# Kernel tuning notes

Measured on AMD Instinct MI355X. Metric: run time of the kernel, lower is better.

Reference implementation:

```python
import jax, jax.numpy as jnp
import numpy as np

L, CIN, CKV, E, H, D, NQ, NK = 3, 128, 256, 128, 8, 16, 4096, 1024
CLAMP_MAX = 65503.0  # torch.clamp(max=65503)
SCALE = 1.0 / (D * D)  # non-standard: 1 / projection_dim**2


def group_norm(x, w, b, groups, eps=1e-5):
    # x: [..., C, N]; w, b broadcastable to x.shape[:-1] (i.e. lead + (C,))
    lead = x.shape[:-2]
    C, N = x.shape[-2:]
    xg = x.reshape(lead + (groups, C // groups, N))
    mu = xg.mean(axis=(-2, -1), keepdims=True)
    var = ((xg - mu) ** 2).mean(axis=(-2, -1), keepdims=True)
    xn = ((xg - mu) * jax.lax.rsqrt(var + eps)).reshape(lead + (C, N))
    return xn * w[..., None] + b[..., None]


def split_heads(t):
    # [L, 1, E, N] -> [L, 1, H, N, D]
    l, b, e, n = t.shape
    return t.transpose(0, 1, 3, 2).reshape(l, b, n, H, D).transpose(0, 1, 3, 2, 4)


def setup_inputs():
    key = jax.random.key(0)
    ks = jax.random.split(key, 18)
    r = lambda k, s: jax.random.normal(k, s, dtype=jnp.float32)
    return {
        'x': r(ks[0], (1, CIN, NQ)),
        'x_global': r(ks[1], (L, CKV, NK)),
        'xyz': r(ks[2], (1, NQ, 3)),
        'xyz_global': r(ks[3], (L, NK, 3)),
        'gn1_w': r(ks[4], (CIN,)), 'gn1_b': r(ks[5], (CIN,)),
        'gn2_w': r(ks[6], (L, CKV)), 'gn2_b': r(ks[7], (L, CKV)),
        'qw': r(ks[8], (L, E, CIN)) * 0.05, 'qb': r(ks[9], (L, E)),
        'kw': r(ks[10], (L, E, CKV)) * 0.05, 'kb': r(ks[11], (L, E)),
        'vw': r(ks[12], (L, E, CKV)) * 0.05, 'vb': r(ks[13], (L, E)),
        'qgn_w': r(ks[14], (L, E)), 'qgn_b': r(ks[15], (L, E)),
        'cw': r(ks[16], (L, CIN, E)) * 0.05, 'cb': r(ks[17], (L, CIN)),
    }


def reference(x, x_global, xyz, xyz_global, gn1_w, gn1_b, gn2_w, gn2_b,
              qw, qb, kw, kb, vw, vb, qgn_w, qgn_b, cw, cb):
    # pre-norm of query features (shared across layers): [1, CIN, NQ]
    xq = jax.nn.relu(group_norm(x, gn1_w, gn1_b, 8))
    # per-source KV features: [L, 1, CKV, NK]
    xg = jax.nn.relu(group_norm(x_global[:, None], gn2_w[:, None], gn2_b[:, None], 16))

    # conv1d (kernel=1) projections + the shared q_gn GroupNorm(8, E)
    q = jnp.einsum('lec,bcn->lben', qw, xq) + qb[:, None, :, None]        # [L,1,E,NQ]
    q = group_norm(q, qgn_w[:, None], qgn_b[:, None], 8)
    k = jnp.einsum('lec,lbcn->lben', kw, xg) + kb[:, None, :, None]       # [L,1,E,NK]
    k = group_norm(k, qgn_w[:, None], qgn_b[:, None], 8)
    v = jnp.einsum('lec,lbcn->lben', vw, xg) + vb[:, None, :, None]       # [L,1,E,NK]
    v = group_norm(v, qgn_w[:, None], qgn_b[:, None], 8)

    qh, kh, vh = split_heads(q), split_heads(k), split_heads(v)           # [L,1,H,*,D]

    score = jnp.einsum('lbhqd,lbhkd->lbhqk', qh * SCALE, kh)              # [L,1,H,NQ,NK]
    score = jnp.minimum(score, CLAMP_MAX)
    w_att = jax.nn.softmax(score, axis=-1)
    o = jnp.einsum('lbhqk,lbhkd->lbhqd', w_att, vh)                        # [L,1,H,NQ,D]
    o = o.transpose(0, 1, 3, 2, 4).reshape(L, 1, NQ, E)                    # merge heads
    o = jnp.einsum('lbqe,loe->lbqo', o, cw) + cb[:, None, None, :]         # combine heads
    o = o.transpose(0, 1, 3, 2) + xq[None]                                 # [L,1,CIN,NQ], SA residual

    out = o.mean(axis=0) + x                                               # mean over sources + block residual
    return out, w_att[-1]                                                  # weight of last layer, as in torch loop
```

## Files before the change

kernel.cpp:

```cpp
#include <hip/hip_runtime.h>
#include <math.h>

constexpr int NQ = 4096, NK = 1024, CIN = 128, CKV = 256, E = 128, H = 8, D = 16, LAYERS = 3;
constexpr float SCALE = 1.0f / 256.0f;
constexpr float CLAMP_MAX = 65503.0f;
constexpr float LOG2E = 1.44269504088896340736f;
constexpr float CLAMP2 = CLAMP_MAX * LOG2E;

typedef __bf16 bf16x8 __attribute__((ext_vector_type(8)));
typedef __bf16 bf16x4 __attribute__((ext_vector_type(4)));
typedef float f32x16 __attribute__((ext_vector_type(16)));
typedef float f32x4 __attribute__((ext_vector_type(4)));

__device__ __forceinline__ float exp2_fast(float x) {
#if __has_builtin(__builtin_amdgcn_exp2f)
  return __builtin_amdgcn_exp2f(x);
#else
  return exp2f(x);
#endif
}

__device__ __forceinline__ void block_reduce2(float& a, float& b, float* red) {
#pragma unroll
  for (int off = 32; off > 0; off >>= 1) {
    a += __shfl_down(a, off, 64);
    b += __shfl_down(b, off, 64);
  }
  int lane = threadIdx.x & 63, wid = threadIdx.x >> 6;
  if (lane == 0) { red[wid * 2] = a; red[wid * 2 + 1] = b; }
  __syncthreads();
  if (threadIdx.x == 0) {
    float sa = 0.f, sb = 0.f;
#pragma unroll
    for (int w = 0; w < 4; w++) { sa += red[w * 2]; sb += red[w * 2 + 1]; }
    red[0] = sa; red[1] = sb;
  }
  __syncthreads();
  a = red[0]; b = red[1];
}

__global__ __launch_bounds__(256) void pre_partial(const float* __restrict__ x,
                                                   const float* __restrict__ xg,
                                                   float* __restrict__ acc) {
  __shared__ float red[8];
  int b = blockIdx.x, t = threadIdx.x;
  const float4* p;
  int aidx;
  if (b < 256) { p = (const float4*)x + (size_t)b * 512; aidx = b >> 5; }
  else { int i = b - 256; p = (const float4*)xg + (size_t)i * 512; aidx = 8 + (i >> 3); }
  float s = 0.f, sq = 0.f;
#pragma unroll
  for (int i = 0; i < 2; i++) {
    float4 v = p[t + i * 256];
    s += v.x + v.y + v.z + v.w;
    sq += v.x * v.x + v.y * v.y + v.z * v.z + v.w * v.w;
  }
  block_reduce2(s, sq, red);
  if (t == 0) {
    atomicAdd(&acc[aidx * 2], s);
    atomicAdd(&acc[aidx * 2 + 1], sq);
  }
}

__global__ __launch_bounds__(256) void stage_a(const float* __restrict__ x,
                                               const float* __restrict__ xg,
                                               const float* __restrict__ acc,
                                               const float* __restrict__ gn1w,
                                               const float* __restrict__ gn1b,
                                               const float* __restrict__ gn2w,
                                               const float* __restrict__ gn2b,
                                               const float* __restrict__ qw,
                                               const float* __restrict__ kw,
                                               const float* __restrict__ vw,
                                               __bf16* __restrict__ xq_t,
                                               __bf16* __restrict__ xg_t,
                                               __bf16* __restrict__ qwb,
                                               __bf16* __restrict__ kwb,
                                               __bf16* __restrict__ vwb) {
  int b = blockIdx.x, t = threadIdx.x;
  if (b >= 320) {
    int i = b - 320;
    const float* src; __bf16* dst; int off;
    if (i < 24)      { src = qw; dst = qwb; off = i * 2048; }
    else if (i < 72) { src = kw; dst = kwb; off = (i - 24) * 2048; }
    else             { src = vw; dst = vwb; off = (i - 72) * 2048; }
    int base = off + t * 8;
    float4 a = *(const float4*)(src + base);
    float4 c = *(const float4*)(src + base + 4);
    bf16x8 o = { (__bf16)a.x, (__bf16)a.y, (__bf16)a.z, (__bf16)a.w,
                 (__bf16)c.x, (__bf16)c.y, (__bf16)c.z, (__bf16)c.w };
    *(bf16x8*)(dst + base) = o;
    return;
  }
  __shared__ float T[128 * 36];
  const float* in; __bf16* out; int N, Cout, ccbase, n0, gbase;
  const float* gw; const float* gb; float inv;
  if (b < 128) {
    in = x; N = NQ; out = xq_t; Cout = 128; ccbase = 0; n0 = b * 32;
    gw = gn1w; gb = gn1b; gbase = 0; inv = 1.f / 65536.f;
  } else {
    int i = b - 128; int l = i / 64; int r = i % 64; int ch = r >> 5;
    n0 = (r & 31) * 32;
    in = xg + ((size_t)l * 256 + ch * 128) * 1024; N = NK;
    out = xg_t + (size_t)l * 1024 * 256; Cout = 256; ccbase = ch * 128;
    gw = gn2w + l * 256 + ch * 128; gb = gn2b + l * 256 + ch * 128;
    gbase = 8 + l * 16 + ch * 8; inv = 1.f / 16384.f;
  }
  int nq = t & 7, cbase = t >> 3;
#pragma unroll
  for (int i = 0; i < 4; i++) {
    int c = cbase + 32 * i;
    int g = gbase + (c >> 4);
    float mu = acc[2 * g] * inv;
    float rs = rsqrtf(acc[2 * g + 1] * inv - mu * mu + 1e-5f);
    float sc = gw[c] * rs, sh = gb[c] - mu * sc;
    float4 v = *(const float4*)(in + (size_t)c * N + n0 + nq * 4);
    float4 o;
    o.x = fmaxf(v.x * sc + sh, 0.f);
    o.y = fmaxf(v.y * sc + sh, 0.f);
    o.z = fmaxf(v.z * sc + sh, 0.f);
    o.w = fmaxf(v.w * sc + sh, 0.f);
    *(float4*)(T + c * 36 + nq * 4) = o;
  }
  __syncthreads();
  int n = t >> 3, c0 = (t & 7) * 16;
  bf16x8 o1, o2;
#pragma unroll
  for (int j = 0; j < 8; j++) {
    o1[j] = (__bf16)T[(c0 + j) * 36 + n];
    o2[j] = (__bf16)T[(c0 + 8 + j) * 36 + n];
  }
  __bf16* op = out + (size_t)(n0 + n) * Cout + ccbase + c0;
  *(bf16x8*)op = o1;
  *(bf16x8*)(op + 8) = o2;
}

template <int KSTEPS>
__device__ __forceinline__ void gemm_tile(const __bf16* __restrict__ A,
                                          const __bf16* __restrict__ Bm,
                                          int stride, f32x16& acc, int l31, int half) {
#pragma unroll
  for (int ks = 0; ks < KSTEPS; ks++) {
    bf16x8 af = *(const bf16x8*)(A + (size_t)l31 * stride + ks * 16 + half * 8);
    bf16x8 bf = *(const bf16x8*)(Bm + (size_t)l31 * stride + ks * 16 + half * 8);
    acc = __builtin_amdgcn_mfma_f32_32x32x16_bf16(af, bf, acc, 0, 0, 0);
  }
}

__global__ __launch_bounds__(256) void proj_mfma(const __bf16* __restrict__ xq_t,
                                                 const __bf16* __restrict__ xg_t,
                                                 const __bf16* __restrict__ qwb,
                                                 const __bf16* __restrict__ kwb,
                                                 const __bf16* __restrict__ vwb,
                                                 const float* __restrict__ qb,
                                                 const float* __restrict__ kb,
                                                 const float* __restrict__ vb,
                                                 __bf16* __restrict__ q_raw,
                                                 __bf16* __restrict__ k_raw,
                                                 __bf16* __restrict__ v_raw,
                                                 float* __restrict__ qgnAcc) {
  int t = threadIdx.x;
  int w = blockIdx.x * 4 + (t >> 6);
  int lane = t & 63, l31 = lane & 31, half = lane >> 5;
  f32x16 acc = {0.f,0.f,0.f,0.f,0.f,0.f,0.f,0.f,0.f,0.f,0.f,0.f,0.f,0.f,0.f,0.f};
  int mat, l, e0, n0, N;
  const __bf16* A; const __bf16* Bm; const float* bias;
  if (w < 1536) {
    mat = 0; l = w >> 9; int r = w & 511; e0 = (r & 3) * 32; n0 = (r >> 2) * 32;
    N = NQ; A = qwb + (size_t)l * 128 * 128; Bm = xq_t; bias = qb + l * 128;
  } else if (w < 1920) {
    mat = 1; int idx = w - 1536; l = idx >> 7; int r = idx & 127;
    e0 = (r & 3) * 32; n0 = (r >> 2) * 32;
    N = NK; A = kwb + (size_t)l * 128 * 256; Bm = xg_t + (size_t)l * 1024 * 256;
    bias = kb + l * 128;
  } else {
    mat = 2; int idx = w - 1920; l = idx >> 7; int r = idx & 127;
    e0 = (r & 3) * 32; n0 = (r >> 2) * 32;
    N = NK; A = vwb + (size_t)l * 128 * 256; Bm = xg_t + (size_t)l * 1024 * 256;
    bias = vb + l * 128;
  }
  if (mat == 0) {
    gemm_tile<8>(A + (size_t)e0 * 128, Bm + (size_t)n0 * 128, 128, acc, l31, half);
  } else {
    gemm_tile<16>(A + (size_t)e0 * 256, Bm + (size_t)n0 * 256, 256, acc, l31, half);
  }

  float vals[16];
  float s0 = 0.f, sq0 = 0.f, s1 = 0.f, sq1 = 0.f;
#pragma unroll
  for (int r = 0; r < 16; r++) {
    int row = (r & 3) + 8 * (r >> 2) + 4 * half;
    float v = acc[r] + bias[e0 + row];
    vals[r] = v;
    if (r < 8) { s0 += v; sq0 += v * v; } else { s1 += v; sq1 += v * v; }
  }
#pragma unroll
  for (int off = 1; off < 64; off <<= 1) {
    s0 += __shfl_xor(s0, off); sq0 += __shfl_xor(sq0, off);
    s1 += __shfl_xor(s1, off); sq1 += __shfl_xor(sq1, off);
  }
  int gbase = (mat == 0 ? 0 : (mat == 1 ? 24 : 48)) + l * 8 + (e0 >> 4);
  if (lane == 0) {
    atomicAdd(&qgnAcc[gbase * 2], s0);
    atomicAdd(&qgnAcc[gbase * 2 + 1], sq0);
    atomicAdd(&qgnAcc[(gbase + 1) * 2], s1);
    atomicAdd(&qgnAcc[(gbase + 1) * 2 + 1], sq1);
  }
  if (mat < 2) {
    __bf16* out = (mat == 0 ? q_raw : k_raw);
#pragma unroll
    for (int qd = 0; qd < 4; qd++) {
      int h = (e0 >> 4) + (qd >> 1);
      int d0 = 4 * half + 8 * (qd & 1);
      bf16x4 o;
#pragma unroll
      for (int j = 0; j < 4; j++) o[j] = (__bf16)vals[qd * 4 + j];
      *(bf16x4*)(out + ((size_t)(l * 8 + h) * N + n0 + l31) * 16 + d0) = o;
    }
  } else {
#pragma unroll
    for (int r = 0; r < 16; r++) {
      int row = (r & 3) + 8 * (r >> 2) + 4 * half;
      int h = (e0 >> 4) + (row >> 4);
      v_raw[((size_t)(l * 8 + h) * 16 + (row & 15)) * NK + n0 + l31] = (__bf16)vals[r];
    }
  }
}

__global__ __launch_bounds__(256) void qkv_affine(__bf16* __restrict__ q_raw,
                                                  __bf16* __restrict__ k_raw,
                                                  __bf16* __restrict__ v_raw,
                                                  const float* __restrict__ acc,
                                                  const float* __restrict__ gw,
                                                  const float* __restrict__ gb) {
  int b = blockIdx.x, t = threadIdx.x;
  if (b < 768) {
    int v8 = b * 256 + t;
    int d0 = (v8 & 1) * 8;
    int lh = (v8 >> 1) >> 12;
    int l = lh >> 3, h = lh & 7;
    int g = l * 8 + h;
    const float inv = 1.f / 65536.f;
    float mu = acc[2 * g] * inv;
    float rs = rsqrtf(acc[2 * g + 1] * inv - mu * mu + 1e-5f);
    const float EX = SCALE * LOG2E;
    bf16x8 vv = *(bf16x8*)(q_raw + (size_t)v8 * 8);
    bf16x8 o;
#pragma unroll
    for (int j = 0; j < 8; j++) {
      int cidx = l * 128 + h * 16 + d0 + j;
      float w0 = gw[cidx] * rs;
      o[j] = (__bf16)(((float)vv[j] * w0 + (gb[cidx] - mu * w0)) * EX);
    }
    *(bf16x8*)(q_raw + (size_t)v8 * 8) = o;
  } else if (b < 960) {
    int v8 = (b - 768) * 256 + t;
    int d0 = (v8 & 1) * 8;
    int lh = (v8 >> 1) >> 10;
    int l = lh >> 3, h = lh & 7;
    int g = 24 + l * 8 + h;
    const float inv = 1.f / 16384.f;
    float mu = acc[2 * g] * inv;
    float rs = rsqrtf(acc[2 * g + 1] * inv - mu * mu + 1e-5f);
    bf16x8 vv = *(bf16x8*)(k_raw + (size_t)v8 * 8);
    bf16x8 o;
#pragma unroll
    for (int j = 0; j < 8; j++) {
      int cidx = l * 128 + h * 16 + d0 + j;
      float w0 = gw[cidx] * rs;
      o[j] = (__bf16)((float)vv[j] * w0 + (gb[cidx] - mu * w0));
    }
    *(bf16x8*)(k_raw + (size_t)v8 * 8) = o;
  } else {
    int v8 = (b - 960) * 256 + t;
    int rest = v8 >> 7;
    int d = rest & 15, lh = rest >> 4;
    int l = lh >> 3, h = lh & 7;
    int g = 48 + l * 8 + h;
    const float inv = 1.f / 16384.f;
    float mu = acc[2 * g] * inv;
    float rs = rsqrtf(acc[2 * g + 1] * inv - mu * mu + 1e-5f);
    int cidx = l * 128 + h * 16 + d;
    float w0 = gw[cidx] * rs;
    float sh = gb[cidx] - mu * w0;
    bf16x8 vv = *(bf16x8*)(v_raw + (size_t)v8 * 8);
    bf16x8 o;
#pragma unroll
    for (int j = 0; j < 8; j++) o[j] = (__bf16)((float)vv[j] * w0 + sh);
    *(bf16x8*)(v_raw + (size_t)v8 * 8) = o;
  }
}

__global__ __launch_bounds__(256) void attn_kernel(const __bf16* __restrict__ qbf,
                                                   const __bf16* __restrict__ kbf,
                                                   const __bf16* __restrict__ vbf,
                                                   float* __restrict__ ob,
                                                   float* __restrict__ wout) {
  __shared__ __bf16 Pt[4][32 * 40];
  __shared__ float rinv_s[4][32];

  const int t = threadIdx.x;
  const int wv = t >> 6;
  const int lane = t & 63;
  const int l31 = lane & 31, half = lane >> 5, l15 = lane & 15, quad = lane >> 4;
  const int h = blockIdx.y, l = blockIdx.z;
  const int q0 = blockIdx.x * 128 + wv * 32;

  const __bf16* Qh = qbf + (size_t)(l * H + h) * NQ * D;
  const __bf16* Kh = kbf + (size_t)(l * H + h) * NK * D;
  const __bf16* Vh = vbf + (size_t)(l * H + h) * D * NK;

  const bf16x8 qfrag = *(const bf16x8*)(Qh + (size_t)(q0 + l31) * D + half * 8);

  f32x4 oa0 = {0.f, 0.f, 0.f, 0.f}, oa1 = {0.f, 0.f, 0.f, 0.f};
  float rsum[16];
#pragma unroll
  for (int r = 0; r < 16; ++r) rsum[r] = 0.f;

  __bf16* Pw = &Pt[wv][0];

  for (int c = 0; c < 32; ++c) {
    const int k0 = c * 32;
    bf16x8 kf = *(const bf16x8*)(Kh + (size_t)(k0 + l31) * D + half * 8);
    f32x16 s = {0.f,0.f,0.f,0.f,0.f,0.f,0.f,0.f,0.f,0.f,0.f,0.f,0.f,0.f,0.f,0.f};
    s = __builtin_amdgcn_mfma_f32_32x32x16_bf16(qfrag, kf, s, 0, 0, 0);
#pragma unroll
    for (int r = 0; r < 16; ++r) {
      float p = exp2_fast(fminf(s[r], CLAMP2));
      rsum[r] += p;
      int row = (r & 3) + 8 * (r >> 2) + 4 * half;
      Pw[row * 40 + l31] = (__bf16)p;
    }
    bf16x8 a0 = *(const bf16x8*)(Pw + l15 * 40 + quad * 8);
    bf16x8 a1 = *(const bf16x8*)(Pw + (16 + l15) * 40 + quad * 8);
    bf16x8 bv = *(const bf16x8*)(Vh + (size_t)l15 * NK + k0 + quad * 8);
    oa0 = __builtin_amdgcn_mfma_f32_16x16x32_bf16(a0, bv, oa0, 0, 0, 0);
    oa1 = __builtin_amdgcn_mfma_f32_16x16x32_bf16(a1, bv, oa1, 0, 0, 0);
  }

#pragma unroll
  for (int r = 0; r < 16; ++r) {
    float v = rsum[r];
    v += __shfl_xor(v, 1); v += __shfl_xor(v, 2); v += __shfl_xor(v, 4);
    v += __shfl_xor(v, 8); v += __shfl_xor(v, 16);
    rsum[r] = v;
  }
  if (l31 == 0) {
#pragma unroll
    for (int r = 0; r < 16; ++r)
      rinv_s[wv][(r & 3) + 8 * (r >> 2) + 4 * half] = 1.f / rsum[r];
  }

  float* Ow = (float*)Pw;
#pragma unroll
  for (int r = 0; r < 4; ++r) {
    int qa = quad * 4 + r;
    Ow[l15 * 36 + qa] = oa0[r] * rinv_s[wv][qa];
    Ow[l15 * 36 + 16 + qa] = oa1[r] * rinv_s[wv][16 + qa];
  }
  {
    int dd = lane >> 2, j = (lane & 3) * 8;
    float4 u0 = *(const float4*)(Ow + dd * 36 + j);
    float4 u1 = *(const float4*)(Ow + dd * 36 + j + 4);
    size_t rb = (size_t)(l * E + h * D + dd) * NQ + q0 + j;
    *(float4*)(ob + rb) = u0;
    *(float4*)(ob + rb + 4) = u1;
  }

  if (l == 2) {
    float riv[16];
#pragma unroll
    for (int r = 0; r < 16; ++r) riv[r] = 1.f / rsum[r];
    for (int c = 0; c < 32; ++c) {
      const int k0 = c * 32;
      bf16x8 kf = *(const bf16x8*)(Kh + (size_t)(k0 + l31) * D + half * 8);
      f32x16 s = {0.f,0.f,0.f,0.f,0.f,0.f,0.f,0.f,0.f,0.f,0.f,0.f,0.f,0.f,0.f,0.f};
      s = __builtin_amdgcn_mfma_f32_32x32x16_bf16(qfrag, kf, s, 0, 0, 0);
#pragma unroll
      for (int r = 0; r < 16; ++r) {
        float p = exp2_fast(fminf(s[r], CLAMP2)) * riv[r];
        int row = (r & 3) + 8 * (r >> 2) + 4 * half;
        wout[(size_t)(h * NQ + q0 + row) * NK + k0 + l31] = p;
      }
    }
  }
}

__global__ __launch_bounds__(256) void combine_kernel(const float* __restrict__ x,
                                                      const float* __restrict__ acc,
                                                      const float* __restrict__ gn1w,
                                                      const float* __restrict__ gn1b,
                                                      const float* __restrict__ ob,
                                                      const float* __restrict__ cw,
                                                      const float* __restrict__ cb,
                                                      float* __restrict__ out) {
  int f = blockIdx.x * 256 + threadIdx.x;
  int n0 = (f & 1023) * 4;
  int c0 = (f >> 10) * 2;
  float4 acc0 = make_float4(0.f, 0.f, 0.f, 0.f);
  float4 acc1 = make_float4(0.f, 0.f, 0.f, 0.f);
  for (int l = 0; l < LAYERS; l++) {
    const float* obl = ob + (size_t)l * E * NQ;
    const float* cwl = cw + (size_t)l * CIN * E;
#pragma unroll 4
    for (int e = 0; e < E; e++) {
      float4 ov = *(const float4*)(obl + (size_t)e * NQ + n0);
      float w0 = cwl[(c0 + 0) * E + e];
      float w1 = cwl[(c0 + 1) * E + e];
      acc0.x += w0 * ov.x; acc0.y += w0 * ov.y; acc0.z += w0 * ov.z; acc0.w += w0 * ov.w;
      acc1.x += w1 * ov.x; acc1.y += w1 * ov.y; acc1.z += w1 * ov.z; acc1.w += w1 * ov.w;
    }
  }
  const float third = 1.f / 3.f;
#pragma unroll
  for (int i = 0; i < 2; i++) {
    int c = c0 + i;
    float4 a = i ? acc1 : acc0;
    float bsum = (cb[c] + cb[CIN + c] + cb[2 * CIN + c]) * third;
    int g = c >> 4;
    const float inv = 1.f / 65536.f;
    float mu = acc[2 * g] * inv;
    float rs = rsqrtf(acc[2 * g + 1] * inv - mu * mu + 1e-5f);
    float sc = gn1w[c] * rs, sh = gn1b[c] - mu * sc;
    size_t off = (size_t)c * NQ + n0;
    float4 xv = *(const float4*)(x + off);
    float4 xqv;
    xqv.x = fmaxf(xv.x * sc + sh, 0.f);
    xqv.y = fmaxf(xv.y * sc + sh, 0.f);
    xqv.z = fmaxf(xv.z * sc + sh, 0.f);
    xqv.w = fmaxf(xv.w * sc + sh, 0.f);
    float4 o;
    o.x = xv.x + xqv.x + a.x * third + bsum;
    o.y = xv.y + xqv.y + a.y * third + bsum;
    o.z = xv.z + xqv.z + a.z * third + bsum;
    o.w = xv.w + xqv.w + a.w * third + bsum;
    *(float4*)(out + off) = o;
  }
}

extern "C" void kernel_launch(void* const* d_in, const int* in_sizes, int n_in,
                              void* d_out, int out_size, void* d_ws, size_t ws_size,
                              hipStream_t stream) {
  (void)in_sizes; (void)n_in; (void)out_size;
  const float* x    = (const float*)d_in[0];
  const float* xgi  = (const float*)d_in[1];
  const float* gn1w = (const float*)d_in[4];
  const float* gn1b = (const float*)d_in[5];
  const float* gn2w = (const float*)d_in[6];
  const float* gn2b = (const float*)d_in[7];
  const float* qw   = (const float*)d_in[8];
  const float* qb   = (const float*)d_in[9];
  const float* kw   = (const float*)d_in[10];
  const float* kb   = (const float*)d_in[11];
  const float* vw   = (const float*)d_in[12];
  const float* vb   = (const float*)d_in[13];
  const float* qgnw = (const float*)d_in[14];
  const float* qgnb = (const float*)d_in[15];
  const float* cw   = (const float*)d_in[16];
  const float* cb   = (const float*)d_in[17];

  float* ws = (float*)d_ws;
  __bf16* xq_t  = (__bf16*)ws;
  __bf16* xg_t  = (__bf16*)(ws + 262144);
  __bf16* qwb   = (__bf16*)(ws + 655360);
  __bf16* kwb   = (__bf16*)(ws + 679936);
  __bf16* vwb   = (__bf16*)(ws + 729088);
  __bf16* q_raw = (__bf16*)(ws + 778240);
  __bf16* k_raw = (__bf16*)(ws + 1564672);
  __bf16* v_raw = (__bf16*)(ws + 1761280);
  float*  ob    = ws + 1957888;
  float*  accAll = ws + 3530752;
  if (ws_size < (size_t)3531008 * sizeof(float)) return;

  float* qgnAcc = accAll + 112;
  float* outp = (float*)d_out;
  float* wout = outp + 524288;

  hipMemsetAsync(accAll, 0, 256 * sizeof(float), stream);

  pre_partial<<<640, 256, 0, stream>>>(x, xgi, accAll);

  stage_a<<<440, 256, 0, stream>>>(x, xgi, accAll, gn1w, gn1b, gn2w, gn2b,
                                   qw, kw, vw, xq_t, xg_t, qwb, kwb, vwb);

  proj_mfma<<<576, 256, 0, stream>>>(xq_t, xg_t, qwb, kwb, vwb, qb, kb, vb,
                                     q_raw, k_raw, v_raw, qgnAcc);

  qkv_affine<<<1152, 256, 0, stream>>>(q_raw, k_raw, v_raw, qgnAcc, qgnw, qgnb);

  attn_kernel<<<dim3(32, 8, 3), 256, 0, stream>>>(q_raw, k_raw, v_raw, ob, wout);

  combine_kernel<<<256, 256, 0, stream>>>(x, accAll, gn1w, gn1b, ob, cw, cb, outp);
}
```

Measured before the change: 307.2 us.

## Split attention-weight output into separate kernel and tile combine via shared memory

The last layer's softmax weight write (128 MB of fp32) moves out of the attention kernel into a dedicated wout_kernel. That kernel uses the row reciprocals stored in workspace, splits the key range across two blocks and uses nontemporal stores. This removes the imbalance where only layer-2 blocks carried the huge write tail. The combine kernel now stages ob tiles in shared memory and reads cw as vectorised float4, improving reuse. The cost is one extra launch, one extra workspace buffer, and recomputing QK for layer 2.

```diff
diff --git a/kernel.cpp b/kernel.cpp
--- a/kernel.cpp
+++ b/kernel.cpp
@@ -295,7 +295,7 @@
                                                    const __bf16* __restrict__ kbf,
                                                    const __bf16* __restrict__ vbf,
                                                    float* __restrict__ ob,
-                                                   float* __restrict__ wout) {
+                                                   float* __restrict__ rinv_ws) {
   __shared__ __bf16 Pt[4][32 * 40];
   __shared__ float rinv_s[4][32];
 
@@ -358,6 +358,8 @@
     Ow[l15 * 36 + qa] = oa0[r] * rinv_s[wv][qa];
     Ow[l15 * 36 + 16 + qa] = oa1[r] * rinv_s[wv][16 + qa];
   }
+  if (l == 2 && lane < 32)
+    rinv_ws[(size_t)h * NQ + q0 + lane] = rinv_s[wv][lane];
   {
     int dd = lane >> 2, j = (lane & 3) * 8;
     float4 u0 = *(const float4*)(Ow + dd * 36 + j);
@@ -366,22 +368,39 @@
     *(float4*)(ob + rb) = u0;
     *(float4*)(ob + rb + 4) = u1;
   }
-
-  if (l == 2) {
-    float riv[16];
-#pragma unroll
-    for (int r = 0; r < 16; ++r) riv[r] = 1.f / rsum[r];
-    for (int c = 0; c < 32; ++c) {
-      const int k0 = c * 32;
-      bf16x8 kf = *(const bf16x8*)(Kh + (size_t)(k0 + l31) * D + half * 8);
-      f32x16 s = {0.f,0.f,0.f,0.f,0.f,0.f,0.f,0.f,0.f,0.f,0.f,0.f,0.f,0.f,0.f,0.f};
-      s = __builtin_amdgcn_mfma_f32_32x32x16_bf16(qfrag, kf, s, 0, 0, 0);
-#pragma unroll
-      for (int r = 0; r < 16; ++r) {
-        float p = exp2_fast(fminf(s[r], CLAMP2)) * riv[r];
-        int row = (r & 3) + 8 * (r >> 2) + 4 * half;
-        wout[(size_t)(h * NQ + q0 + row) * NK + k0 + l31] = p;
-      }
+}
+
+__global__ __launch_bounds__(256) void wout_kernel(const __bf16* __restrict__ qbf,
+                                                   const __bf16* __restrict__ kbf,
+                                                   const float* __restrict__ rinv_ws,
+                                                   float* __restrict__ wout) {
+  const int t = threadIdx.x;
+  const int wv = t >> 6;
+  const int lane = t & 63;
+  const int l31 = lane & 31, half = lane >> 5;
+  const int h = blockIdx.y;
+  const int q0 = blockIdx.x * 128 + wv * 32;
+  const int kbase = blockIdx.z * 512;
+
+  const __bf16* Qh = qbf + (size_t)(2 * H + h) * NQ * D;
+  const __bf16* Kh = kbf + (size_t)(2 * H + h) * NK * D;
+  const bf16x8 qfrag = *(const bf16x8*)(Qh + (size_t)(q0 + l31) * D + half * 8);
+
+  float riv[16];
+#pragma unroll
+  for (int r = 0; r < 16; ++r)
+    riv[r] = rinv_ws[(size_t)h * NQ + q0 + (r & 3) + 8 * (r >> 2) + 4 * half];
+
+  for (int c = 0; c < 16; ++c) {
+    const int k0 = kbase + c * 32;
+    bf16x8 kf = *(const bf16x8*)(Kh + (size_t)(k0 + l31) * D + half * 8);
+    f32x16 s = {0.f,0.f,0.f,0.f,0.f,0.f,0.f,0.f,0.f,0.f,0.f,0.f,0.f,0.f,0.f,0.f};
+    s = __builtin_amdgcn_mfma_f32_32x32x16_bf16(qfrag, kf, s, 0, 0, 0);
+#pragma unroll
+    for (int r = 0; r < 16; ++r) {
+      float p = exp2_fast(fminf(s[r], CLAMP2)) * riv[r];
+      int row = (r & 3) + 8 * (r >> 2) + 4 * half;
+      __builtin_nontemporal_store(p, &wout[(size_t)(h * NQ + q0 + row) * NK + k0 + l31]);
     }
   }
 }
@@ -394,46 +413,61 @@
                                                       const float* __restrict__ cw,
                                                       const float* __restrict__ cb,
                                                       float* __restrict__ out) {
-  int f = blockIdx.x * 256 + threadIdx.x;
-  int n0 = (f & 1023) * 4;
-  int c0 = (f >> 10) * 2;
-  float4 acc0 = make_float4(0.f, 0.f, 0.f, 0.f);
-  float4 acc1 = make_float4(0.f, 0.f, 0.f, 0.f);
+  __shared__ float S[128 * 16];
+  const int t = threadIdx.x;
+  const int nt0 = blockIdx.x * 16;
+  const int c0 = (t >> 2) * 2;
+  const int nf = t & 3;
+  float4 a0 = make_float4(0.f, 0.f, 0.f, 0.f);
+  float4 a1 = make_float4(0.f, 0.f, 0.f, 0.f);
   for (int l = 0; l < LAYERS; l++) {
-    const float* obl = ob + (size_t)l * E * NQ;
+    if (l) __syncthreads();
+#pragma unroll
+    for (int i = 0; i < 2; i++) {
+      int fid = i * 256 + t;
+      int e = fid >> 2, pos = fid & 3;
+      *(float4*)(S + e * 16 + pos * 4) =
+          *(const float4*)(ob + ((size_t)l * E + e) * NQ + nt0 + pos * 4);
+    }
+    __syncthreads();
     const float* cwl = cw + (size_t)l * CIN * E;
-#pragma unroll 4
-    for (int e = 0; e < E; e++) {
-      float4 ov = *(const float4*)(obl + (size_t)e * NQ + n0);
-      float w0 = cwl[(c0 + 0) * E + e];
-      float w1 = cwl[(c0 + 1) * E + e];
-      acc0.x += w0 * ov.x; acc0.y += w0 * ov.y; acc0.z += w0 * ov.z; acc0.w += w0 * ov.w;
-      acc1.x += w1 * ov.x; acc1.y += w1 * ov.y; acc1.z += w1 * ov.z; acc1.w += w1 * ov.w;
+#pragma unroll 8
+    for (int e4 = 0; e4 < E / 4; e4++) {
+      const int e = e4 * 4;
+      float4 w0 = *(const float4*)(cwl + (size_t)c0 * E + e);
+      float4 w1 = *(const float4*)(cwl + (size_t)(c0 + 1) * E + e);
+      float4 s0 = *(const float4*)(S + (e + 0) * 16 + nf * 4);
+      float4 s1 = *(const float4*)(S + (e + 1) * 16 + nf * 4);
+      float4 s2 = *(const float4*)(S + (e + 2) * 16 + nf * 4);
+      float4 s3 = *(const float4*)(S + (e + 3) * 16 + nf * 4);
+      a0.x += w0.x * s0.x + w0.y * s1.x + w0.z * s2.x + w0.w * s3.x;
+      a0.y += w0.x * s0.y + w0.y * s1.y + w0.z * s2.y + w0.w * s3.y;
+      a0.z += w0.x * s0.z + w0.y * s1.z + w0.z * s2.z + w0.w * s3.z;
+      a0.w += w0.x * s0.w + w0.y * s1.w + w0.z * s2.w + w0.w * s3.w;
+      a1.x += w1.x * s0.x + w1.y * s1.x + w1.z * s2.x + w1.w * s3.x;
+      a1.y += w1.x * s0.y + w1.y * s1.y + w1.z * s2.y + w1.w * s3.y;
+      a1.z += w1.x * s0.z + w1.y * s1.z + w1.z * s2.z + w1.w * s3.z;
+      a1.w += w1.x * s0.w + w1.y * s1.w + w1.z * s2.w + w1.w * s3.w;
     }
   }
   const float third = 1.f / 3.f;
 #pragma unroll
   for (int i = 0; i < 2; i++) {
     int c = c0 + i;
-    float4 a = i ? acc1 : acc0;
+    float4 a = i ? a1 : a0;
     float bsum = (cb[c] + cb[CIN + c] + cb[2 * CIN + c]) * third;
     int g = c >> 4;
     const float inv = 1.f / 65536.f;
     float mu = acc[2 * g] * inv;
     float rs = rsqrtf(acc[2 * g + 1] * inv - mu * mu + 1e-5f);
     float sc = gn1w[c] * rs, sh = gn1b[c] - mu * sc;
-    size_t off = (size_t)c * NQ + n0;
+    size_t off = (size_t)c * NQ + nt0 + nf * 4;
     float4 xv = *(const float4*)(x + off);
-    float4 xqv;
-    xqv.x = fmaxf(xv.x * sc + sh, 0.f);
-    xqv.y = fmaxf(xv.y * sc + sh, 0.f);
-    xqv.z = fmaxf(xv.z * sc + sh, 0.f);
-    xqv.w = fmaxf(xv.w * sc + sh, 0.f);
     float4 o;
-    o.x = xv.x + xqv.x + a.x * third + bsum;
-    o.y = xv.y + xqv.y + a.y * third + bsum;
-    o.z = xv.z + xqv.z + a.z * third + bsum;
-    o.w = xv.w + xqv.w + a.w * third + bsum;
+    o.x = xv.x + fmaxf(xv.x * sc + sh, 0.f) + a.x * third + bsum;
+    o.y = xv.y + fmaxf(xv.y * sc + sh, 0.f) + a.y * third + bsum;
+    o.z = xv.z + fmaxf(xv.z * sc + sh, 0.f) + a.z * third + bsum;
+    o.w = xv.w + fmaxf(xv.w * sc + sh, 0.f) + a.w * third + bsum;
     *(float4*)(out + off) = o;
   }
 }
@@ -470,7 +504,8 @@
   __bf16* v_raw = (__bf16*)(ws + 1761280);
   float*  ob    = ws + 1957888;
   float*  accAll = ws + 3530752;
-  if (ws_size < (size_t)3531008 * sizeof(float)) return;
+  float*  rinv_ws = ws + 3531008;
+  if (ws_size < (size_t)3563776 * sizeof(float)) return;
 
   float* qgnAcc = accAll + 112;
   float* outp = (float*)d_out;
@@ -488,7 +523,9 @@
 
   qkv_affine<<<1152, 256, 0, stream>>>(q_raw, k_raw, v_raw, qgnAcc, qgnw, qgnb);
 
-  attn_kernel<<<dim3(32, 8, 3), 256, 0, stream>>>(q_raw, k_raw, v_raw, ob, wout);
+  attn_kernel<<<dim3(32, 8, 3), 256, 0, stream>>>(q_raw, k_raw, v_raw, ob, rinv_ws);
 
   combine_kernel<<<256, 256, 0, stream>>>(x, accAll, gn1w, gn1b, ob, cw, cb, outp);
-}
+
+  wout_kernel<<<dim3(32, 8, 2), 256, 0, stream>>>(q_raw, k_raw, rinv_ws, wout);
+}
```

Result: no change. 302.3 us (-1.6%).
